# Kernel optimization log

Measured on AMD Instinct MI355X. Metric: run time of the kernel, lower is better.

Reference implementation:

```python
import jax, jax.numpy as jnp
import numpy as np

N_HEAD, D_MODEL, D_K, D_V = 8, 512, 64, 64
WINDOW, THRESH = 2, 0.5
TEMP = float(np.sqrt(D_K))
LN_EPS = 1e-5


def setup_inputs() -> dict:
    key = jax.random.key(0)
    ks = jax.random.split(key, 12)
    B, L = 4, 2048
    std_qk = np.sqrt(2.0 / (D_MODEL + D_K))
    std_v = np.sqrt(2.0 / (D_MODEL + D_V))
    return {
        "q": jax.random.normal(ks[0], (B, L, D_MODEL), jnp.float32),
        "k": jax.random.normal(ks[1], (B, L, D_MODEL), jnp.float32),
        "v": jax.random.normal(ks[2], (B, L, D_MODEL), jnp.float32),
        "w_q": jax.random.normal(ks[3], (N_HEAD * D_K, D_MODEL), jnp.float32) * std_qk,
        "b_q": jnp.zeros((N_HEAD * D_K,), jnp.float32),
        "w_k": jax.random.normal(ks[4], (N_HEAD * D_K, D_MODEL), jnp.float32) * std_qk,
        "b_k": jnp.zeros((N_HEAD * D_K,), jnp.float32),
        "w_v": jax.random.normal(ks[5], (N_HEAD * D_V, D_MODEL), jnp.float32) * std_v,
        "b_v": jnp.zeros((N_HEAD * D_V,), jnp.float32),
        "w_g": jax.random.normal(ks[6], (1, D_K), jnp.float32) * (1.0 / np.sqrt(D_K)),
        "b_g": jnp.zeros((1,), jnp.float32),
        "w_fc": jax.random.normal(ks[7], (D_MODEL, N_HEAD * D_V), jnp.float32) * (1.0 / np.sqrt(D_MODEL)),
        "b_fc": jnp.zeros((D_MODEL,), jnp.float32),
        "ln_g": jnp.ones((D_MODEL,), jnp.float32),
        "ln_b": jnp.zeros((D_MODEL,), jnp.float32),
    }


def reference(q, k, v, w_q, b_q, w_k, b_k, w_v, b_v, w_g, b_g, w_fc, b_fc, ln_g, ln_b):
    B, Lq, _ = q.shape
    Lk = k.shape[1]
    residual = q
    # project and split heads: (h, B, L, d)
    qh = (q @ w_q.T + b_q).reshape(B, Lq, N_HEAD, D_K).transpose(2, 0, 1, 3)
    kh = (k @ w_k.T + b_k).reshape(B, Lk, N_HEAD, D_K).transpose(2, 0, 1, 3)
    vh = (v @ w_v.T + b_v).reshape(B, Lk, N_HEAD, D_V).transpose(2, 0, 1, 3)

    scores = jnp.einsum('hbqd,hbkd->hbqk', qh, kh) / TEMP  # (h, B, Lq, Lk)

    # dynamic gate: tokens with sigmoid(gate) > THRESH keep full attention,
    # others are restricted to a +/-WINDOW sliding window
    gate_open = jax.nn.sigmoid(jnp.einsum('hbqd,od->hbqo', qh, w_g) + b_g)[..., 0] > THRESH
    i = jnp.arange(Lq)[:, None]
    j = jnp.arange(Lk)[None, :]
    win = jnp.abs(i - j) <= WINDOW  # (Lq, Lk)
    allowed = gate_open[..., None] | win  # (h, B, Lq, Lk)
    scores = jnp.where(allowed, scores, -jnp.inf)

    attn = jax.nn.softmax(scores, axis=-1)  # dropout is identity in eval
    out = jnp.einsum('hbqk,hbkd->hbqd', attn, vh)
    out = out.transpose(1, 2, 0, 3).reshape(B, Lq, N_HEAD * D_V)
    out = out @ w_fc.T + b_fc

    x = out + residual
    mu = jnp.mean(x, axis=-1, keepdims=True)
    var = jnp.mean((x - mu) ** 2, axis=-1, keepdims=True)
    out = (x - mu) * jax.lax.rsqrt(var + LN_EPS) * ln_g + ln_b

    return out, attn.reshape(N_HEAD * B, Lq, Lk)
```

## Files before the change

kernel.cpp:

```cpp
#include <hip/hip_runtime.h>


typedef _Float16 f16;
typedef _Float16 f16x8 __attribute__((ext_vector_type(8)));
typedef _Float16 f16x4 __attribute__((ext_vector_type(4)));
typedef float f32x4 __attribute__((ext_vector_type(4)));

#define OUT0_ELEMS (4 * 2048 * 512)
#define QSCALE 0.1803368801111204f

__device__ __forceinline__ f16x8 cvt8(float4 a, float4 b) {
  f16x8 r;
  r[0] = (f16)a.x; r[1] = (f16)a.y; r[2] = (f16)a.z; r[3] = (f16)a.w;
  r[4] = (f16)b.x; r[5] = (f16)b.y; r[6] = (f16)b.z; r[7] = (f16)b.w;
  return r;
}

__device__ __forceinline__ void bar_lds() {
  asm volatile("s_waitcnt lgkmcnt(0)" ::: "memory");
  __builtin_amdgcn_s_barrier();
}

__global__ __launch_bounds__(256) void prep_kernel(
    const float* __restrict__ w_q, const float* __restrict__ b_q,
    const float* __restrict__ w_g, const float* __restrict__ b_g,
    double* __restrict__ wge, double* __restrict__ bqg) {
  int idx = blockIdx.x * 256 + threadIdx.x;
  if (idx < 4096) {
    int h = idx >> 9, c = idx & 511;
    double acc = 0.0;
    for (int d = 0; d < 64; ++d)
      acc += (double)w_g[d] * (double)w_q[(h * 64 + d) * 512 + c];
    wge[idx] = acc;
  }
  if (idx < 8) {
    double acc = (double)b_g[0];
    for (int d = 0; d < 64; ++d)
      acc += (double)b_q[idx * 64 + d] * (double)w_g[d];
    bqg[idx] = acc;
  }
}

__global__ __launch_bounds__(256) void gate_kernel(
    const float* __restrict__ q, const double* __restrict__ wge,
    const double* __restrict__ bqg, int* __restrict__ gate) {
  int lane = threadIdx.x & 63, wid = threadIdx.x >> 6;
  int tok = blockIdx.x * 4 + wid;
  int b = tok >> 11, l = tok & 2047;
  const float* qr = q + (long)tok * 512;
  float qv[8];
#pragma unroll
  for (int j = 0; j < 8; ++j) qv[j] = qr[lane + 64 * j];
#pragma unroll
  for (int h = 0; h < 8; ++h) {
    double acc = 0.0;
#pragma unroll
    for (int j = 0; j < 8; ++j) acc += (double)qv[j] * wge[h * 512 + lane + 64 * j];
#pragma unroll
    for (int off = 1; off < 64; off <<= 1) acc += __shfl_xor(acc, off);
    double logit = acc + bqg[h];
    if (lane == 0) gate[(h * 4 + b) * 2048 + l] = (logit > 0.0) ? 1 : 0;
  }
}

__global__ __launch_bounds__(256) void compact_kernel(
    const int* __restrict__ gate, unsigned short* __restrict__ perm,
    int* __restrict__ nopen) {
  __shared__ int wsum[4];
  const int hb = blockIdx.x, t = threadIdx.x;
  const int lane = t & 63, wid = t >> 6;
  const int base = hb * 2048;
  int g[8];
  int cnt = 0;
#pragma unroll
  for (int i = 0; i < 8; ++i) { g[i] = gate[base + t * 8 + i]; cnt += g[i]; }
  int inc = cnt;
#pragma unroll
  for (int off = 1; off < 64; off <<= 1) {
    int y = __shfl_up(inc, off);
    if (lane >= off) inc += y;
  }
  if (lane == 63) wsum[wid] = inc;
  __syncthreads();
  int wbase = 0;
  for (int w = 0; w < wid; ++w) wbase += wsum[w];
  const int totOpen = wsum[0] + wsum[1] + wsum[2] + wsum[3];
  int openPos = wbase + inc - cnt;
  int closedPos = totOpen + t * 8 - openPos;
#pragma unroll
  for (int i = 0; i < 8; ++i) {
    int l = t * 8 + i;
    if (g[i]) perm[base + openPos++] = (unsigned short)l;
    else      perm[base + closedPos++] = (unsigned short)l;
  }
  if (t == 0) nopen[hb] = totOpen;
}

template <int EPI>
__global__ __launch_bounds__(256) void gemm512(
    const float* __restrict__ A, const float* __restrict__ W,
    const float* __restrict__ bias, const float* __restrict__ res,
    f16* __restrict__ out16, float* __restrict__ outf, float oscale) {
  __shared__ __align__(16) f16 As[64 * 32];
  __shared__ __align__(16) f16 Ws[64 * 32];
  const int tid = threadIdx.x;
  const int lane = tid & 63, wid = tid >> 6;
  const int lo = lane & 15, hi = lane >> 4;
  const int m0 = blockIdx.x * 64, n0 = blockIdx.y * 64;
  const int wm = wid >> 1, wn = wid & 1;

  const int srow = tid >> 2, sseg = tid & 3;
  const int ssu = sseg ^ (srow & 3);
  const float* gA = A + (long)(m0 + srow) * 512 + sseg * 8;
  const float* gW = W + (long)(n0 + srow) * 512 + sseg * 8;
  f16* wA = &As[srow * 32 + ssu * 8];
  f16* wW = &Ws[srow * 32 + ssu * 8];

  const f32x4 zero4 = {0.f, 0.f, 0.f, 0.f};
  f32x4 acc[2][2] = {{zero4, zero4}, {zero4, zero4}};
  const int ra0 = wm * 32 + lo;
  const int rb0 = wn * 32 + lo;
  const int sa = hi ^ (ra0 & 3);
  const int sb = hi ^ (rb0 & 3);

  for (int kk = 0; kk < 512; kk += 32) {
    float4 a0 = *(const float4*)(gA + kk);
    float4 a1 = *(const float4*)(gA + kk + 4);
    float4 w0 = *(const float4*)(gW + kk);
    float4 w1 = *(const float4*)(gW + kk + 4);
    *(f16x8*)wA = cvt8(a0, a1);
    *(f16x8*)wW = cvt8(w0, w1);
    __syncthreads();
    f16x8 af0 = *(const f16x8*)&As[ra0 * 32 + sa * 8];
    f16x8 af1 = *(const f16x8*)&As[(ra0 + 16) * 32 + sa * 8];
    f16x8 bf0 = *(const f16x8*)&Ws[rb0 * 32 + sb * 8];
    f16x8 bf1 = *(const f16x8*)&Ws[(rb0 + 16) * 32 + sb * 8];
    acc[0][0] = __builtin_amdgcn_mfma_f32_16x16x32_f16(af0, bf0, acc[0][0], 0, 0, 0);
    acc[0][1] = __builtin_amdgcn_mfma_f32_16x16x32_f16(af0, bf1, acc[0][1], 0, 0, 0);
    acc[1][0] = __builtin_amdgcn_mfma_f32_16x16x32_f16(af1, bf0, acc[1][0], 0, 0, 0);
    acc[1][1] = __builtin_amdgcn_mfma_f32_16x16x32_f16(af1, bf1, acc[1][1], 0, 0, 0);
    __syncthreads();
  }

#pragma unroll
  for (int i = 0; i < 2; ++i)
#pragma unroll
    for (int j = 0; j < 2; ++j)
#pragma unroll
      for (int r = 0; r < 4; ++r) {
        const int m = m0 + wm * 32 + i * 16 + hi * 4 + r;
        const int n = n0 + wn * 32 + j * 16 + lo;
        float v = (acc[i][j][r] + bias[n]) * oscale;
        if constexpr (EPI == 0) {
          const int b = m >> 11, l = m & 2047, h = n >> 6, d = n & 63;
          out16[(long)((h * 4 + b) * 2048 + l) * 64 + d] = (f16)v;
        } else if constexpr (EPI == 2) {
          const int b = m >> 11, l = m & 2047, h = n >> 6, d = n & 63;
          out16[(long)((h * 4 + b) * 64 + d) * 2048 + l] = (f16)v;
        } else {
          outf[(long)m * 512 + n] = v + res[(long)m * 512 + n];
        }
      }
}

__device__ __forceinline__ uint4 ldK512(const f16* __restrict__ g, int tid) {
  return *(const uint4*)(g + tid * 8);
}
__device__ __forceinline__ uint4 ldV512(const f16* __restrict__ g, int tid) {
  return *(const uint4*)(g + (long)(tid >> 3) * 2048 + ((tid & 7) << 3));
}
__device__ __forceinline__ void stW512(uint4 s, f16* lds, int tid) {
  const int row = tid >> 3, seg = tid & 7, sw = row & 7;
  *(uint4*)&lds[(row << 6) + ((seg ^ sw) << 3)] = s;
}

__global__ __launch_bounds__(512) void attn_kernel(
    const f16* __restrict__ qh, const f16* __restrict__ kh,
    const f16* __restrict__ vt, const int* __restrict__ gate,
    const unsigned short* __restrict__ perm, const int* __restrict__ nopen,
    float* __restrict__ attn, float* __restrict__ o) {
  __shared__ __align__(16) f16 Ks[2][4096];
  __shared__ __align__(16) f16 Vs[2][4096];
  __shared__ __align__(16) f16 Ps[8][1024];
  const int tid = threadIdx.x;
  const int lane = tid & 63, wid = tid >> 6;
  const int bid = blockIdx.x;

  if (bid >= 512) {
    const int vb = bid - 512;
    const int xcd = vb & 7, sub = vb >> 3;
    const int hb = xcd * 4 + (sub >> 5);
    const int chunk = sub & 31;
    const int nop = nopen[hb];
    const int j0 = ((nop + 127) & ~127) + (chunk << 6);
    if (j0 >= 2048) return;
    unsigned short* rowIdx = (unsigned short*)&Ks[0][0];
    if (tid < 64) rowIdx[tid] = perm[hb * 2048 + j0 + tid];
    __syncthreads();
    float* abase = attn + ((long)hb * 2048 << 11);
    const f32x4 zero4 = {0.f, 0.f, 0.f, 0.f};
    for (int it = 0; it < 64; ++it)
      *(f32x4*)(abase + ((long)rowIdx[it] << 11) + (tid << 2)) = zero4;
    __syncthreads();
    const f16* qhb = qh + (long)hb * 2048 * 64;
    const f16* khb = kh + (long)hb * 2048 * 64;
    const f16* vtb = vt + (long)hb * 64 * 2048;
    const int b = hb & 3, h = hb >> 2;
    for (int rr = 0; rr < 8; ++rr) {
      const int row = rowIdx[(wid << 3) + rr];
      const int jlo = max(row - 2, 0), jhi = min(row + 2, 2047);
      const float qv = (float)qhb[(long)row * 64 + lane];
      float p0, p1, p2, p3, p4, sum = 0.f;
#pragma unroll
      for (int jj = 0; jj < 5; ++jj) {
        const int j = jlo + jj;
        const int js = min(j, 2047);
        float prod = qv * (float)khb[(long)js * 64 + lane];
        prod += __shfl_xor(prod, 1);
        prod += __shfl_xor(prod, 2);
        prod += __shfl_xor(prod, 4);
        prod += __shfl_xor(prod, 8);
        prod += __shfl_xor(prod, 16);
        prod += __shfl_xor(prod, 32);
        const float e = (j <= jhi) ? exp2f(prod) : 0.f;
        if (jj == 0) p0 = e; else if (jj == 1) p1 = e; else if (jj == 2) p2 = e;
        else if (jj == 3) p3 = e; else p4 = e;
        sum += e;
      }
      const float inv = 1.f / sum;
      float pv = p0;
      pv = (lane == 1) ? p1 : pv;
      pv = (lane == 2) ? p2 : pv;
      pv = (lane == 3) ? p3 : pv;
      pv = (lane == 4) ? p4 : pv;
      if (lane < 5 && (jlo + lane) <= jhi)
        abase[((long)row << 11) + jlo + lane] = pv * inv;
      float od = 0.f;
      od += p0 * (float)vtb[(long)lane * 2048 + min(jlo + 0, 2047)];
      od += p1 * (float)vtb[(long)lane * 2048 + min(jlo + 1, 2047)];
      od += p2 * (float)vtb[(long)lane * 2048 + min(jlo + 2, 2047)];
      od += p3 * (float)vtb[(long)lane * 2048 + min(jlo + 3, 2047)];
      od += p4 * (float)vtb[(long)lane * 2048 + min(jlo + 4, 2047)];
      o[(long)(b * 2048 + row) * 512 + (h << 6) + lane] = od * inv;
    }
    return;
  }

  const int lo = lane & 15, hi = lane >> 4;
  const int xcd = bid & 7, local = bid >> 3;
  const int hb = xcd * 4 + (local >> 4);
  const int q0 = (local & 15) << 7;
  const int nop = nopen[hb];
  if (q0 >= nop) return;
  const bool fullopen = (q0 + 128 <= nop);

  const unsigned short* pm = perm + hb * 2048 + q0;
  const f16* khb = kh + (long)hb * 2048 * 64;
  const f16* vtb = vt + (long)hb * 64 * 2048;

  const int rowA = pm[(wid << 4) + lo];
  const f16* qrow = qh + (long)(hb * 2048 + rowA) * 64;
  const f16x8 aq0 = *(const f16x8*)(qrow + (hi << 3));
  const f16x8 aq1 = *(const f16x8*)(qrow + 32 + (hi << 3));

  int qi[4], gt[4];
  float psum[4];
#pragma unroll
  for (int r = 0; r < 4; ++r) {
    qi[r] = pm[(wid << 4) + (hi << 2) + r];
    gt[r] = gate[hb * 2048 + qi[r]];
    psum[r] = 0.f;
  }
  const f32x4 zero4 = {0.f, 0.f, 0.f, 0.f};

  {
    uint4 kreg = ldK512(khb, tid);
    stW512(kreg, &Ks[0][0], tid);
    kreg = ldK512(khb + 4096, tid);
    int cur = 0;
    for (int kt = 0; kt < 32; ++kt) {
      bar_lds();
      if (kt < 31) {
        stW512(kreg, &Ks[cur ^ 1][0], tid);
        if (kt < 30) kreg = ldK512(khb + (long)(kt + 2) * 4096, tid);
      }
      const f16* Kc = &Ks[cur][0];
      f32x4 sacc[4] = {zero4, zero4, zero4, zero4};
      __builtin_amdgcn_s_setprio(1);
#pragma unroll
      for (int s = 0; s < 2; ++s) {
        const f16x8 aa = s ? aq1 : aq0;
#pragma unroll
        for (int nt = 0; nt < 4; ++nt) {
          const int krow = (nt << 4) + lo;
          const f16x8 b = *(const f16x8*)&Kc[(krow << 6) + ((((s << 2) + hi) ^ (krow & 7)) << 3)];
          sacc[nt] = __builtin_amdgcn_mfma_f32_16x16x32_f16(aa, b, sacc[nt], 0, 0, 0);
        }
      }
      __builtin_amdgcn_s_setprio(0);
      if (fullopen) {
#pragma unroll
        for (int nt = 0; nt < 4; ++nt)
#pragma unroll
          for (int r = 0; r < 4; ++r) psum[r] += exp2f(sacc[nt][r]);
      } else {
        const int kkb = (kt << 6) + lo;
#pragma unroll
        for (int nt = 0; nt < 4; ++nt) {
          const int kk = kkb + (nt << 4);
#pragma unroll
          for (int r = 0; r < 4; ++r) {
            const bool allowed = gt[r] || ((unsigned)(kk - qi[r] + 2) <= 4u);
            psum[r] += allowed ? exp2f(sacc[nt][r]) : 0.f;
          }
        }
      }
      cur ^= 1;
    }
  }

  float invl[4];
#pragma unroll
  for (int r = 0; r < 4; ++r) {
    float s = psum[r];
    s += __shfl_xor(s, 1);
    s += __shfl_xor(s, 2);
    s += __shfl_xor(s, 4);
    s += __shfl_xor(s, 8);
    invl[r] = 1.f / s;
  }

  f32x4 oacc[4] = {zero4, zero4, zero4, zero4};
  f16* Pw = &Ps[wid][0];
  const int row2 = lane >> 2, qq = lane & 3;
  float* arow = attn + ((long)(hb * 2048 + pm[(wid << 4) + row2]) << 11);

  {
    uint4 kreg = ldK512(khb, tid);
    uint4 vreg = ldV512(vtb, tid);
    stW512(kreg, &Ks[0][0], tid);
    stW512(vreg, &Vs[0][0], tid);
    kreg = ldK512(khb + 4096, tid);
    vreg = ldV512(vtb + 64, tid);
    int cur = 0;
    for (int kt = 0; kt < 32; ++kt) {
      bar_lds();
      if (kt < 31) {
        stW512(kreg, &Ks[cur ^ 1][0], tid);
        stW512(vreg, &Vs[cur ^ 1][0], tid);
        if (kt < 30) {
          kreg = ldK512(khb + (long)(kt + 2) * 4096, tid);
          vreg = ldV512(vtb + ((kt + 2) << 6), tid);
        }
      }
      const f16* Kc = &Ks[cur][0];
      const f16* Vc = &Vs[cur][0];
      f32x4 sacc[4] = {zero4, zero4, zero4, zero4};
      __builtin_amdgcn_s_setprio(1);
#pragma unroll
      for (int s = 0; s < 2; ++s) {
        const f16x8 aa = s ? aq1 : aq0;
#pragma unroll
        for (int nt = 0; nt < 4; ++nt) {
          const int krow = (nt << 4) + lo;
          const f16x8 b = *(const f16x8*)&Kc[(krow << 6) + ((((s << 2) + hi) ^ (krow & 7)) << 3)];
          sacc[nt] = __builtin_amdgcn_mfma_f32_16x16x32_f16(aa, b, sacc[nt], 0, 0, 0);
        }
      }
      __builtin_amdgcn_s_setprio(0);
      if (fullopen) {
#pragma unroll
        for (int nt = 0; nt < 4; ++nt)
#pragma unroll
          for (int r = 0; r < 4; ++r) {
            const float p = exp2f(sacc[nt][r]) * invl[r];
            const int prow = (hi << 2) + r;
            const int pcol = (nt << 4) + lo;
            Pw[(prow << 6) + (((pcol >> 3) ^ (prow & 7)) << 3) + (pcol & 7)] = (f16)p;
          }
      } else {
        const int kkb = (kt << 6) + lo;
#pragma unroll
        for (int nt = 0; nt < 4; ++nt) {
          const int kk = kkb + (nt << 4);
#pragma unroll
          for (int r = 0; r < 4; ++r) {
            const bool allowed = gt[r] || ((unsigned)(kk - qi[r] + 2) <= 4u);
            const float p = allowed ? exp2f(sacc[nt][r]) * invl[r] : 0.f;
            const int prow = (hi << 2) + r;
            const int pcol = (nt << 4) + lo;
            Pw[(prow << 6) + (((pcol >> 3) ^ (prow & 7)) << 3) + (pcol & 7)] = (f16)p;
          }
        }
      }
      __builtin_amdgcn_s_setprio(1);
#pragma unroll
      for (int s = 0; s < 2; ++s) {
        const f16x8 ap = *(const f16x8*)&Pw[(lo << 6) + ((((s << 2) + hi) ^ (lo & 7)) << 3)];
#pragma unroll
        for (int nt = 0; nt < 4; ++nt) {
          const int vrow = (nt << 4) + lo;
          const f16x8 bv = *(const f16x8*)&Vc[(vrow << 6) + ((((s << 2) + hi) ^ (vrow & 7)) << 3)];
          oacc[nt] = __builtin_amdgcn_mfma_f32_16x16x32_f16(ap, bv, oacc[nt], 0, 0, 0);
        }
      }
      __builtin_amdgcn_s_setprio(0);
      {
        const int swz = row2 & 7;
        float* dst = arow + (kt << 6) + (qq << 2);
#pragma unroll
        for (int i = 0; i < 4; ++i) {
          const f16x4 pv = *(const f16x4*)&Pw[(row2 << 6) + ((((i << 1) + (qq >> 1)) ^ swz) << 3) + ((qq & 1) << 2)];
          f32x4 fo = {(float)pv[0], (float)pv[1], (float)pv[2], (float)pv[3]};
          *(f32x4*)(dst + (i << 4)) = fo;
        }
      }
      cur ^= 1;
    }
  }

  const int b = hb & 3, h = hb >> 2;
#pragma unroll
  for (int nt = 0; nt < 4; ++nt)
#pragma unroll
    for (int r = 0; r < 4; ++r)
      o[(long)(b * 2048 + qi[r]) * 512 + (h << 6) + (nt << 4) + lo] = oacc[nt][r];
}

__global__ __launch_bounds__(256) void ln_kernel(float* __restrict__ x,
                                                 const float* __restrict__ g,
                                                 const float* __restrict__ bta) {
  __shared__ float red[8];
  const int t = threadIdx.x;
  float* row = x + (long)blockIdx.x * 512;
  float v0 = row[t], v1 = row[t + 256];
  float s = v0 + v1;
#pragma unroll
  for (int off = 1; off < 64; off <<= 1) s += __shfl_xor(s, off);
  if ((t & 63) == 0) red[t >> 6] = s;
  __syncthreads();
  const float mean = (red[0] + red[1] + red[2] + red[3]) * (1.f / 512.f);
  const float d0 = v0 - mean, d1 = v1 - mean;
  float sq = d0 * d0 + d1 * d1;
#pragma unroll
  for (int off = 1; off < 64; off <<= 1) sq += __shfl_xor(sq, off);
  if ((t & 63) == 0) red[4 + (t >> 6)] = sq;
  __syncthreads();
  const float var = (red[4] + red[5] + red[6] + red[7]) * (1.f / 512.f);
  const float rstd = 1.f / sqrtf(var + 1e-5f);
  row[t] = d0 * rstd * g[t] + bta[t];
  row[t + 256] = d1 * rstd * g[t + 256] + bta[t + 256];
}

extern "C" void kernel_launch(void* const* d_in, const int* in_sizes, int n_in,
                              void* d_out, int out_size, void* d_ws, size_t ws_size,
                              hipStream_t stream) {
  const float* q    = (const float*)d_in[0];
  const float* k    = (const float*)d_in[1];
  const float* v    = (const float*)d_in[2];
  const float* w_q  = (const float*)d_in[3];
  const float* b_q  = (const float*)d_in[4];
  const float* w_k  = (const float*)d_in[5];
  const float* b_k  = (const float*)d_in[6];
  const float* w_v  = (const float*)d_in[7];
  const float* b_v  = (const float*)d_in[8];
  const float* w_g  = (const float*)d_in[9];
  const float* b_g  = (const float*)d_in[10];
  const float* w_fc = (const float*)d_in[11];
  const float* b_fc = (const float*)d_in[12];
  const float* ln_g = (const float*)d_in[13];
  const float* ln_b = (const float*)d_in[14];

  char* wsb = (char*)d_ws;
  f16* qh16   = (f16*)wsb;
  f16* kh16   = qh16 + 4194304;
  f16* vt16   = kh16 + 4194304;
  float* ob   = (float*)(wsb + 25165824);
  int* gateb  = (int*)(wsb + 25165824 + 16777216);
  double* wge = (double*)(wsb + 25165824 + 16777216 + 262144);
  double* bqg = wge + 4096;
  unsigned short* permb = (unsigned short*)(wsb + 25165824 + 16777216 + 262144 + 32768 + 64);
  int* nopenb = (int*)(wsb + 25165824 + 16777216 + 262144 + 32768 + 64 + 131072);

  float* out0 = (float*)d_out;
  float* attn = out0 + OUT0_ELEMS;

  prep_kernel<<<16, 256, 0, stream>>>(w_q, b_q, w_g, b_g, wge, bqg);
  gate_kernel<<<2048, 256, 0, stream>>>(q, wge, bqg, gateb);
  compact_kernel<<<32, 256, 0, stream>>>(gateb, permb, nopenb);

  dim3 gp(128, 8);
  gemm512<0><<<gp, 256, 0, stream>>>(q, w_q, b_q, nullptr, qh16, nullptr, QSCALE);
  gemm512<0><<<gp, 256, 0, stream>>>(k, w_k, b_k, nullptr, kh16, nullptr, 1.0f);
  gemm512<2><<<gp, 256, 0, stream>>>(v, w_v, b_v, nullptr, vt16, nullptr, 1.0f);

  attn_kernel<<<1536, 512, 0, stream>>>(qh16, kh16, vt16, gateb, permb, nopenb, attn, ob);

  gemm512<3><<<gp, 256, 0, stream>>>(ob, w_fc, b_fc, q, nullptr, out0, 1.0f);
  ln_kernel<<<8192, 256, 0, stream>>>(out0, ln_g, ln_b);
}
```

Before: 272.6 us.

## Fuse gate logit computation into Q projection GEMM and remap blocks per XCD

Removes the separate gate kernel by computing the double-precision gate logit inside the Q projection GEMM. The GEMM already loads each q row tile there, so this saves a full re-read of q. Each of the 8 column blocks (one per head) accumulates its head's gate dot product using the folded w_g·w_q vector and writes the gate flag. All GEMMs also switch to a 1D grid with an XCD-aware block-to-tile mapping, so consecutive rows on the same XCD share L2. The cost is extra double-precision math in the Q GEMM's inner loop.

```diff
diff --git a/kernel.cpp b/kernel.cpp
--- a/kernel.cpp
+++ b/kernel.cpp
@@ -41,28 +41,6 @@
   }
 }
 
-__global__ __launch_bounds__(256) void gate_kernel(
-    const float* __restrict__ q, const double* __restrict__ wge,
-    const double* __restrict__ bqg, int* __restrict__ gate) {
-  int lane = threadIdx.x & 63, wid = threadIdx.x >> 6;
-  int tok = blockIdx.x * 4 + wid;
-  int b = tok >> 11, l = tok & 2047;
-  const float* qr = q + (long)tok * 512;
-  float qv[8];
-#pragma unroll
-  for (int j = 0; j < 8; ++j) qv[j] = qr[lane + 64 * j];
-#pragma unroll
-  for (int h = 0; h < 8; ++h) {
-    double acc = 0.0;
-#pragma unroll
-    for (int j = 0; j < 8; ++j) acc += (double)qv[j] * wge[h * 512 + lane + 64 * j];
-#pragma unroll
-    for (int off = 1; off < 64; off <<= 1) acc += __shfl_xor(acc, off);
-    double logit = acc + bqg[h];
-    if (lane == 0) gate[(h * 4 + b) * 2048 + l] = (logit > 0.0) ? 1 : 0;
-  }
-}
-
 __global__ __launch_bounds__(256) void compact_kernel(
     const int* __restrict__ gate, unsigned short* __restrict__ perm,
     int* __restrict__ nopen) {
@@ -100,13 +78,18 @@
 __global__ __launch_bounds__(256) void gemm512(
     const float* __restrict__ A, const float* __restrict__ W,
     const float* __restrict__ bias, const float* __restrict__ res,
-    f16* __restrict__ out16, float* __restrict__ outf, float oscale) {
+    f16* __restrict__ out16, float* __restrict__ outf, float oscale,
+    const double* __restrict__ wge, const double* __restrict__ bqg,
+    int* __restrict__ gate) {
   __shared__ __align__(16) f16 As[64 * 32];
   __shared__ __align__(16) f16 Ws[64 * 32];
   const int tid = threadIdx.x;
   const int lane = tid & 63, wid = tid >> 6;
   const int lo = lane & 15, hi = lane >> 4;
-  const int m0 = blockIdx.x * 64, n0 = blockIdx.y * 64;
+  const int bid = blockIdx.x;
+  const int xcd = bid & 7, s = bid >> 3;
+  const int m0 = (xcd * 16 + (s >> 3)) * 64;
+  const int n0 = (s & 7) * 64;
   const int wm = wid >> 1, wn = wid & 1;
 
   const int srow = tid >> 2, sseg = tid & 3;
@@ -122,12 +105,20 @@
   const int rb0 = wn * 32 + lo;
   const int sa = hi ^ (ra0 & 3);
   const int sb = hi ^ (rb0 & 3);
+  double gacc = 0.0;
 
   for (int kk = 0; kk < 512; kk += 32) {
     float4 a0 = *(const float4*)(gA + kk);
     float4 a1 = *(const float4*)(gA + kk + 4);
     float4 w0 = *(const float4*)(gW + kk);
     float4 w1 = *(const float4*)(gW + kk + 4);
+    if constexpr (EPI == 1) {
+      const double* wg = wge + (n0 << 3) + kk + sseg * 8;
+      gacc += (double)a0.x * wg[0] + (double)a0.y * wg[1] +
+              (double)a0.z * wg[2] + (double)a0.w * wg[3] +
+              (double)a1.x * wg[4] + (double)a1.y * wg[5] +
+              (double)a1.z * wg[6] + (double)a1.w * wg[7];
+    }
     *(f16x8*)wA = cvt8(a0, a1);
     *(f16x8*)wW = cvt8(w0, w1);
     __syncthreads();
@@ -142,6 +133,17 @@
     __syncthreads();
   }
 
+  if constexpr (EPI == 1) {
+    gacc += __shfl_xor(gacc, 1);
+    gacc += __shfl_xor(gacc, 2);
+    if (sseg == 0) {
+      const int h = n0 >> 6;
+      const int m = m0 + srow, b = m >> 11, l = m & 2047;
+      const double logit = gacc + bqg[h];
+      gate[(h * 4 + b) * 2048 + l] = (logit > 0.0) ? 1 : 0;
+    }
+  }
+
 #pragma unroll
   for (int i = 0; i < 2; ++i)
 #pragma unroll
@@ -151,7 +153,7 @@
         const int m = m0 + wm * 32 + i * 16 + hi * 4 + r;
         const int n = n0 + wn * 32 + j * 16 + lo;
         float v = (acc[i][j][r] + bias[n]) * oscale;
-        if constexpr (EPI == 0) {
+        if constexpr (EPI <= 1) {
           const int b = m >> 11, l = m & 2047, h = n >> 6, d = n & 63;
           out16[(long)((h * 4 + b) * 2048 + l) * 64 + d] = (f16)v;
         } else if constexpr (EPI == 2) {
@@ -486,16 +488,14 @@
   float* attn = out0 + OUT0_ELEMS;
 
   prep_kernel<<<16, 256, 0, stream>>>(w_q, b_q, w_g, b_g, wge, bqg);
-  gate_kernel<<<2048, 256, 0, stream>>>(q, wge, bqg, gateb);
+
+  gemm512<1><<<1024, 256, 0, stream>>>(q, w_q, b_q, nullptr, qh16, nullptr, QSCALE, wge, bqg, gateb);
   compact_kernel<<<32, 256, 0, stream>>>(gateb, permb, nopenb);
-
-  dim3 gp(128, 8);
-  gemm512<0><<<gp, 256, 0, stream>>>(q, w_q, b_q, nullptr, qh16, nullptr, QSCALE);
-  gemm512<0><<<gp, 256, 0, stream>>>(k, w_k, b_k, nullptr, kh16, nullptr, 1.0f);
-  gemm512<2><<<gp, 256, 0, stream>>>(v, w_v, b_v, nullptr, vt16, nullptr, 1.0f);
+  gemm512<0><<<1024, 256, 0, stream>>>(k, w_k, b_k, nullptr, kh16, nullptr, 1.0f, nullptr, nullptr, nullptr);
+  gemm512<2><<<1024, 256, 0, stream>>>(v, w_v, b_v, nullptr, vt16, nullptr, 1.0f, nullptr, nullptr, nullptr);
 
   attn_kernel<<<1536, 512, 0, stream>>>(qh16, kh16, vt16, gateb, permb, nopenb, attn, ob);
 
-  gemm512<3><<<gp, 256, 0, stream>>>(ob, w_fc, b_fc, q, nullptr, out0, 1.0f);
+  gemm512<3><<<1024, 256, 0, stream>>>(ob, w_fc, b_fc, q, nullptr, out0, 1.0f, nullptr, nullptr, nullptr);
   ln_kernel<<<8192, 256, 0, stream>>>(out0, ln_g, ln_b);
 }
```

Result: no change. 272.2 us (-0.1%).
